# Optimization experiments

Hardware: AMD Instinct MI355X
Metric: run time of the kernel (lower is better)

## Reference

```python
import jax, jax.numpy as jnp
import numpy as np

S, L, K = 4, 256, 32          # num_states, seq length, neighbors
ORIG_H, EMB_H, EXV, RANK = 128, 256, 384, 16


def _integrate(x, Wq, Wk, seq_idx, emb_idx, hidden, rank):
    """AttentionIntegrator.forward: QK^T softmax -> double mean -> softmax -> weighted pool of raw x."""
    x = jnp.moveaxis(x, (seq_idx, emb_idx), (-2, -1))
    orig_shape = x.shape
    Ls = orig_shape[-2]
    xf = x.reshape(-1, Ls, hidden)               # (B, Ls, hidden)
    B = xf.shape[0]
    q = (xf @ Wq.T).reshape(B, Ls, rank, hidden)  # head_dim == hidden
    k = (xf @ Wk.T).reshape(B, Ls, rank, hidden)
    scale = 1.0 / jnp.sqrt(jnp.asarray(hidden, xf.dtype))
    scores = jnp.einsum('blhd,bmhd->bhlm', q, k) * scale
    attn = jax.nn.softmax(scores, axis=-1)        # (B, rank, Ls, Ls)
    w = jax.nn.softmax(attn.mean(axis=(1, 2)), axis=-1)  # (B, Ls)
    pooled = jnp.einsum('bl,bld->bd', w, xf)      # (B, hidden)
    return (pooled.reshape(*orig_shape[:-2], hidden),
            w.reshape(*orig_shape[:-2], Ls))


def setup_inputs() -> dict:
    key = jax.random.key(0)
    ks = jax.random.split(key, 12)
    sc = lambda fan_in: 1.0 / np.sqrt(fan_in)
    return {
        'h_V':    jax.random.normal(ks[0], (S, L, ORIG_H), jnp.float32),
        'h_EXV':  jax.random.normal(ks[1], (S, L, K, EXV), jnp.float32),
        'W_hV':   jax.random.normal(ks[2], (EMB_H, ORIG_H), jnp.float32) * sc(ORIG_H),
        'b_hV':   jnp.zeros((EMB_H,), jnp.float32),
        'Wq_hv':  jax.random.normal(ks[3], (RANK * EMB_H, EMB_H), jnp.float32) * sc(EMB_H),
        'Wk_hv':  jax.random.normal(ks[4], (RANK * EMB_H, EMB_H), jnp.float32) * sc(EMB_H),
        'Wq_ce':  jax.random.normal(ks[5], (RANK * EXV, EXV), jnp.float32) * sc(EXV),
        'Wk_ce':  jax.random.normal(ks[6], (RANK * EXV, EXV), jnp.float32) * sc(EXV),
        'W_ce':   jax.random.normal(ks[7], (EMB_H, EXV), jnp.float32) * sc(EXV),
        'b_ce':   jnp.zeros((EMB_H,), jnp.float32),
        'Wq_sce': jax.random.normal(ks[8], (RANK * EMB_H, EMB_H), jnp.float32) * sc(EMB_H),
        'Wk_sce': jax.random.normal(ks[9], (RANK * EMB_H, EMB_H), jnp.float32) * sc(EMB_H),
    }


def reference(h_V, h_EXV, W_hV, b_hV, Wq_hv, Wk_hv, Wq_ce, Wk_ce, W_ce, b_ce, Wq_sce, Wk_sce):
    # diffmodel.get_weights
    hv = h_V @ W_hV.T + b_hV                                  # (S, L, EMB_H)
    h_V_int, h_V_w = _integrate(hv, Wq_hv, Wk_hv, 0, 2, EMB_H, RANK)   # pool over states
    # chemical environment: pool over k neighbors per (state, position)
    ce, _local_w = _integrate(h_EXV, Wq_ce, Wk_ce, 2, 3, EXV, RANK)    # (S, L, EXV)
    ce = ce @ W_ce.T + b_ce                                   # (S, L, EMB_H)
    ce_int, ce_w = _integrate(ce, Wq_sce, Wk_sce, 0, 2, EMB_H, RANK)   # pool over states
    return (h_V_int[None], h_V_w[None], ce_int[None], ce_w[None])
```

## Files before the change

kernel.cpp:

```cpp
#include <hip/hip_runtime.h>

typedef _Float16 f16;
typedef _Float16 f16x8 __attribute__((ext_vector_type(8)));
typedef _Float16 f16x4 __attribute__((ext_vector_type(4)));
typedef float f32x4 __attribute__((ext_vector_type(4)));

#define MFMA16(a, b, c) __builtin_amdgcn_mfma_f32_16x16x32_f16(a, b, c, 0, 0, 0)
#define MFMA16K16(a, b, c) __builtin_amdgcn_mfma_f32_16x16x16f16(a, b, c, 0, 0, 0)

__global__ __launch_bounds__(256) void k_mt(const float* __restrict__ Wq,
                                            const float* __restrict__ Wk,
                                            f16* __restrict__ MT, int H) {
    const int h = blockIdx.x;
    const int ntile = H >> 6;
    const int nkk = H >> 5;
    const int frow = (blockIdx.y / ntile) * 64;
    const int ecol = (blockIdx.y % ntile) * 64;
    const int t = threadIdx.x;
    const int lane = t & 63;
    const int w = t >> 6;
    const int wr = w >> 1, wc = w & 1;

    __shared__ __align__(16) f16 As[64][40];
    __shared__ __align__(16) f16 Ks[64][40];

    f32x4 acc[2][2] = {};
    const int d = t >> 3;
    const int e8 = (t & 7) * 8;

    for (int kk = 0; kk < nkk; ++kk) {
        const float* gq = Wq + (size_t)(h * H + kk * 32 + d) * H + ecol + e8;
        const float* gk = Wk + (size_t)(h * H + kk * 32 + d) * H + frow + e8;
        float q[8], k[8];
#pragma unroll
        for (int i = 0; i < 8; ++i) { q[i] = gq[i]; k[i] = gk[i]; }
        __syncthreads();
#pragma unroll
        for (int i = 0; i < 8; ++i) { As[e8 + i][d] = (f16)q[i]; Ks[e8 + i][d] = (f16)k[i]; }
        __syncthreads();
        f16x8 a[2], b[2];
#pragma unroll
        for (int rt = 0; rt < 2; ++rt)
            a[rt] = *(const f16x8*)&Ks[wr * 32 + rt * 16 + (lane & 15)][(lane >> 4) * 8];
#pragma unroll
        for (int nt = 0; nt < 2; ++nt)
            b[nt] = *(const f16x8*)&As[wc * 32 + nt * 16 + (lane & 15)][(lane >> 4) * 8];
#pragma unroll
        for (int rt = 0; rt < 2; ++rt)
#pragma unroll
            for (int nt = 0; nt < 2; ++nt)
                acc[rt][nt] = MFMA16(a[rt], b[nt], acc[rt][nt]);
    }
#pragma unroll
    for (int rt = 0; rt < 2; ++rt)
#pragma unroll
        for (int nt = 0; nt < 2; ++nt)
#pragma unroll
            for (int j = 0; j < 4; ++j) {
                int f = frow + wr * 32 + rt * 16 + (lane >> 4) * 4 + j;
                int e = ecol + wc * 32 + nt * 16 + (lane & 15);
                MT[(((size_t)h * nkk + (e >> 5)) * H + f) * 32 + (e & 31)] = (f16)acc[rt][nt][j];
            }
}

__global__ __launch_bounds__(256) void k_lin(const float* __restrict__ in,
                                             const float* __restrict__ W,
                                             const float* __restrict__ bias,
                                             float* __restrict__ out, int K) {
    const int t = threadIdx.x;
    const int r0 = blockIdx.x * 4;
    __shared__ float ins[4][384];
    __shared__ float Ws[256][33];
#pragma unroll
    for (int r = 0; r < 4; ++r)
        for (int off = t; off < K; off += 256)
            ins[r][off] = in[(size_t)(r0 + r) * K + off];
    float acc[4] = {};
    for (int d0 = 0; d0 < K; d0 += 32) {
        __syncthreads();
        for (int i = t; i < 256 * 32; i += 256) {
            int j = i >> 5, dd = i & 31;
            Ws[j][dd] = W[(size_t)j * K + d0 + dd];
        }
        __syncthreads();
#pragma unroll 8
        for (int dd = 0; dd < 32; ++dd) {
            float wv = Ws[t][dd];
#pragma unroll
            for (int r = 0; r < 4; ++r) acc[r] += wv * ins[r][d0 + dd];
        }
    }
    float bv = bias[t];
#pragma unroll
    for (int r = 0; r < 4; ++r) out[(size_t)(r0 + r) * 256 + t] = acc[r] + bv;
}

__global__ __launch_bounds__(256) void k_small_int(const float* __restrict__ X,
                                                   const f16* __restrict__ MT,
                                                   float* __restrict__ wpart) {
    const int t = threadIdx.x;
    const int lane = t & 63;
    const int w = t >> 6;
    const int g = lane >> 4;
    const int l15 = lane & 15;
    const int pos0 = blockIdx.x * 4;
    const int h = blockIdx.y;

    __shared__ __align__(16) f16 Xs[16][264];
    __shared__ __align__(16) f16 Ts[16][264];

    {
        int row = t >> 4, d0 = (t & 15) * 16;
        int s = row & 3, p = row >> 2;
        const float* gx = X + (size_t)(s * 256 + pos0 + p) * 256 + d0;
#pragma unroll
        for (int i = 0; i < 16; i += 8) {
            float4 v0 = *(const float4*)(gx + i);
            float4 v1 = *(const float4*)(gx + i + 4);
            f16x8 o;
            o[0] = (f16)v0.x; o[1] = (f16)v0.y; o[2] = (f16)v0.z; o[3] = (f16)v0.w;
            o[4] = (f16)v1.x; o[5] = (f16)v1.y; o[6] = (f16)v1.z; o[7] = (f16)v1.w;
            *(f16x8*)&Xs[row][d0 + i] = o;
        }
    }
    __syncthreads();

    const f16* mh = MT + (size_t)h * 8 * 256 * 32;
    const int fb = w * 64 + l15;
    f32x4 acc[4] = {};
    f16x8 bq[4], bn[4];
#pragma unroll
    for (int nt = 0; nt < 4; ++nt)
        bq[nt] = *(const f16x8*)(mh + (size_t)(fb + nt * 16) * 32 + g * 8);
#pragma unroll
    for (int kk = 0; kk < 8; ++kk) {
        if (kk < 7) {
#pragma unroll
            for (int nt = 0; nt < 4; ++nt)
                bn[nt] = *(const f16x8*)(mh + ((size_t)(kk + 1) * 256 + fb + nt * 16) * 32 + g * 8);
        }
        f16x8 a = *(const f16x8*)&Xs[l15][kk * 32 + g * 8];
#pragma unroll
        for (int nt = 0; nt < 4; ++nt) acc[nt] = MFMA16(a, bq[nt], acc[nt]);
#pragma unroll
        for (int nt = 0; nt < 4; ++nt) bq[nt] = bn[nt];
    }
#pragma unroll
    for (int nt = 0; nt < 4; ++nt)
#pragma unroll
        for (int j = 0; j < 4; ++j)
            Ts[g * 4 + j][w * 64 + nt * 16 + l15] = (f16)acc[nt][j];
    __syncthreads();

    f32x4 sacc = {};
#pragma unroll
    for (int ks = 0; ks < 8; ++ks) {
        f16x8 a = *(const f16x8*)&Ts[l15][ks * 32 + g * 8];
        f16x8 b = *(const f16x8*)&Xs[l15][ks * 32 + g * 8];
        sacc = MFMA16(a, b, sacc);
    }
    if (w == 0 && (l15 >> 2) == g) {
        const float scale = 1.0f / 16.0f;
        float add = 0.f;
#pragma unroll
        for (int j = 0; j < 4; ++j) {
            float v = sacc[j] * scale;
            float m = v;
            m = fmaxf(m, __shfl_xor(m, 1));
            m = fmaxf(m, __shfl_xor(m, 2));
            float e = expf(v - m);
            float s2 = e;
            s2 += __shfl_xor(s2, 1);
            s2 += __shfl_xor(s2, 2);
            add += e / s2;
        }
        int pg = pos0 + g;
        wpart[((size_t)h * 256 + pg) * 4 + (l15 & 3)] = add;
    }
}

__global__ __launch_bounds__(256) void k_small_fin(const float* __restrict__ wpart,
                                                   const float* __restrict__ X,
                                                   float* __restrict__ out_int,
                                                   float* __restrict__ out_w) {
    const int pos = blockIdx.x, t = threadIdx.x;
    __shared__ float red[64];
    __shared__ float ws[4];
    if (t < 64) red[t] = wpart[((size_t)(t >> 2) * 256 + pos) * 4 + (t & 3)];
    __syncthreads();
    if (t == 0) {
        float v[4];
#pragma unroll
        for (int s = 0; s < 4; ++s) {
            float x = 0.f;
            for (int hh = 0; hh < 16; ++hh) x += red[hh * 4 + s];
            v[s] = x * (1.0f / 64.0f);
        }
        float m = fmaxf(fmaxf(v[0], v[1]), fmaxf(v[2], v[3]));
        float sum = 0.f;
#pragma unroll
        for (int s = 0; s < 4; ++s) { v[s] = expf(v[s] - m); sum += v[s]; }
#pragma unroll
        for (int s = 0; s < 4; ++s) ws[s] = v[s] / sum;
    }
    __syncthreads();
    if (t < 4) out_w[pos * 4 + t] = ws[t];
    float v = 0.f;
#pragma unroll
    for (int s = 0; s < 4; ++s) v += ws[s] * X[(size_t)(s * 256 + pos) * 256 + t];
    out_int[(size_t)pos * 256 + t] = v;
}

#define BUF_OFF 98304

__global__ __launch_bounds__(512, 2) void k_ce_int(const float* __restrict__ Xg32,
                                                   const f16* __restrict__ MT,
                                                   float* __restrict__ acc_out) {
    const int t = threadIdx.x;
    const int lane = t & 63;
    const int w = t >> 6;
    const int g = lane >> 4;
    const int l15 = lane & 15;
    const int bg = blockIdx.x;

    extern __shared__ __align__(16) char smem[];
    char* BUF = smem + BUF_OFF;

    {
        const float* xg = Xg32 + (size_t)bg * 128 * 384;
#pragma unroll
        for (int p = 0; p < 12; ++p) {
            int idx = p * 512 + t;
            int row = idx / 48, s = idx - row * 48;
            int c = s ^ (row & 7);
            const float* src = xg + row * 384 + c * 8;
            float4 v0 = *(const float4*)src;
            float4 v1 = *(const float4*)(src + 4);
            f16x8 o;
            o[0] = (f16)v0.x; o[1] = (f16)v0.y; o[2] = (f16)v0.z; o[3] = (f16)v0.w;
            o[4] = (f16)v1.x; o[5] = (f16)v1.y; o[6] = (f16)v1.z; o[7] = (f16)v1.w;
            *(f16x8*)(smem + idx * 16) = o;
        }
    }
    __syncthreads();

    const f16* mall = MT;
    const int frow = w * 48 + l15;

    f16x8 A[3][3];
#pragma unroll
    for (int ft = 0; ft < 3; ++ft) {
        A[0][ft] = *(const f16x8*)(mall + (size_t)(frow + ft * 16) * 32 + g * 8);
        A[1][ft] = *(const f16x8*)(mall + (size_t)12288 + (size_t)(frow + ft * 16) * 32 + g * 8);
    }

    for (int hi = 0; hi < 16; ++hi) {
        f32x4 acc[3][8] = {};
#pragma unroll
        for (int kk = 0; kk < 12; ++kk) {
            {
                int step = hi * 12 + kk + 2;
                int ns = step < 192 ? step : 191;
#pragma unroll
                for (int ft = 0; ft < 3; ++ft)
                    A[(kk + 2) % 3][ft] =
                        *(const f16x8*)(mall + (size_t)ns * 12288 + (size_t)(frow + ft * 16) * 32 + g * 8);
            }
            f16x8 xb[8];
#pragma unroll
            for (int mt = 0; mt < 8; ++mt) {
                int row = mt * 16 + l15;
                int ch = kk * 4 + g;
                xb[mt] = *(const f16x8*)(smem + row * 768 + ((ch ^ (row & 7)) << 4));
            }
            __builtin_amdgcn_s_setprio(1);
#pragma unroll
            for (int ft = 0; ft < 3; ++ft)
#pragma unroll
                for (int mt = 0; mt < 8; ++mt)
                    acc[ft][mt] = MFMA16(A[kk % 3][ft], xb[mt], acc[ft][mt]);
            __builtin_amdgcn_s_setprio(0);
        }

        f16x4 bf[3][8];
#pragma unroll
        for (int ft = 0; ft < 3; ++ft)
#pragma unroll
            for (int mt = 0; mt < 8; ++mt) {
                f32x4 v = acc[ft][mt];
                f16x4 o;
                o[0] = (f16)v[0]; o[1] = (f16)v[1]; o[2] = (f16)v[2]; o[3] = (f16)v[3];
                bf[ft][mt] = o;
            }

#pragma unroll
        for (int r = 0; r < 2; ++r) {
            f32x4 s2[2][2][2] = {};
#pragma unroll
            for (int bb = 0; bb < 2; ++bb) {
                const int b = 2 * r + bb;
#pragma unroll
                for (int ks = 0; ks < 3; ++ks)
#pragma unroll
                    for (int it = 0; it < 2; ++it) {
                        int row = b * 32 + it * 16 + l15;
                        int ch = 6 * w + 2 * ks + (g >> 1);
                        f16x4 av = *(const f16x4*)(smem + row * 768 +
                                                   ((ch ^ (row & 7)) << 4) + 8 * (g & 1));
#pragma unroll
                        for (int lt = 0; lt < 2; ++lt)
                            s2[bb][it][lt] = MFMA16K16(av, bf[ks][2 * b + lt], s2[bb][it][lt]);
                    }
            }
#pragma unroll
            for (int bb = 0; bb < 2; ++bb)
#pragma unroll
                for (int it = 0; it < 2; ++it)
#pragma unroll
                    for (int lt = 0; lt < 2; ++lt)
                        *(f32x4*)(BUF + w * 8192 + (bb * 4 + it * 2 + lt) * 1024 + lane * 16) =
                            s2[bb][it][lt];
            __syncthreads();

            if ((w >> 2) == r) {
                const int wl = w & 3;
                const int bb = wl >> 1;
                const int it = wl & 1;
                const int b = 2 * r + bb;
                f32x4 sum0 = {0.f, 0.f, 0.f, 0.f};
                f32x4 sum1 = {0.f, 0.f, 0.f, 0.f};
#pragma unroll
                for (int src = 0; src < 8; ++src) {
                    const char* pb = BUF + src * 8192 + (bb * 4 + it * 2) * 1024 + lane * 16;
                    sum0 += *(const f32x4*)pb;
                    sum1 += *(const f32x4*)(pb + 1024);
                }
                const float scale = 0.051031036307982884f;
                float cs0 = 0.f, cs1 = 0.f;
#pragma unroll
                for (int j = 0; j < 4; ++j) {
                    float v0 = sum0[j] * scale, v1 = sum1[j] * scale;
                    float m = fmaxf(v0, v1);
                    m = fmaxf(m, __shfl_xor(m, 1));
                    m = fmaxf(m, __shfl_xor(m, 2));
                    m = fmaxf(m, __shfl_xor(m, 4));
                    m = fmaxf(m, __shfl_xor(m, 8));
                    float e0 = expf(v0 - m), e1 = expf(v1 - m);
                    float s = e0 + e1;
                    s += __shfl_xor(s, 1);
                    s += __shfl_xor(s, 2);
                    s += __shfl_xor(s, 4);
                    s += __shfl_xor(s, 8);
                    float inv = 1.f / s;
                    cs0 += e0 * inv;
                    cs1 += e1 * inv;
                }
                cs0 += __shfl_xor(cs0, 16); cs0 += __shfl_xor(cs0, 32);
                cs1 += __shfl_xor(cs1, 16); cs1 += __shfl_xor(cs1, 32);
                if (lane < 16) {
                    float* o = acc_out + (((size_t)hi * 1024 + bg * 4 + b) * 2 + it) * 32;
                    o[l15] = cs0;
                    o[16 + l15] = cs1;
                }
            }
            __syncthreads();
        }
    }
}

__global__ __launch_bounds__(128) void k_ce_pool(const float* __restrict__ accp,
                                                 const float* __restrict__ exv,
                                                 float* __restrict__ pooled) {
    const int b = blockIdx.x;
    const int t = threadIdx.x;
    __shared__ float wm[32];
    __shared__ float ww[32];
    if (t < 32) {
        float s = 0.f;
#pragma unroll
        for (int h = 0; h < 16; ++h) {
            s += accp[(((size_t)h * 1024 + b) * 2 + 0) * 32 + t];
            s += accp[(((size_t)h * 1024 + b) * 2 + 1) * 32 + t];
        }
        wm[t] = s * (1.0f / 512.0f);
    }
    __syncthreads();
    if (t == 0) {
        float m = wm[0];
        for (int i = 1; i < 32; ++i) m = fmaxf(m, wm[i]);
        float s = 0.f;
        for (int i = 0; i < 32; ++i) { float e = expf(wm[i] - m); ww[i] = e; s += e; }
        float inv = 1.f / s;
        for (int i = 0; i < 32; ++i) ww[i] *= inv;
    }
    __syncthreads();
    for (int d = t; d < 384; d += 128) {
        float v = 0.f;
#pragma unroll
        for (int m = 0; m < 32; ++m) v += ww[m] * exv[((size_t)b * 32 + m) * 384 + d];
        pooled[(size_t)b * 384 + d] = v;
    }
}

extern "C" void kernel_launch(void* const* d_in, const int* in_sizes, int n_in,
                              void* d_out, int out_size, void* d_ws, size_t ws_size,
                              hipStream_t stream) {
    const float* h_V    = (const float*)d_in[0];
    const float* h_EXV  = (const float*)d_in[1];
    const float* W_hV   = (const float*)d_in[2];
    const float* b_hV   = (const float*)d_in[3];
    const float* Wq_hv  = (const float*)d_in[4];
    const float* Wk_hv  = (const float*)d_in[5];
    const float* Wq_ce  = (const float*)d_in[6];
    const float* Wk_ce  = (const float*)d_in[7];
    const float* W_ce   = (const float*)d_in[8];
    const float* b_ce   = (const float*)d_in[9];
    const float* Wq_sce = (const float*)d_in[10];
    const float* Wk_sce = (const float*)d_in[11];
    float* out = (float*)d_out;

    char* ws = (char*)d_ws;
    f16*   mt_hv  = (f16*)(ws + 0);
    f16*   mt_sce = (f16*)(ws + 2097152);
    f16*   mt_ce  = (f16*)(ws + 4194304);
    float* hv     = (float*)(ws + 8912896);
    float* ce     = (float*)(ws + 9961472);
    float* accp   = (float*)(ws + 11010048);
    float* pooled = (float*)(ws + 15204352);
    float* wpart  = accp;

    k_mt<<<dim3(16, 16), 256, 0, stream>>>(Wq_hv, Wk_hv, mt_hv, 256);
    k_mt<<<dim3(16, 36), 256, 0, stream>>>(Wq_ce, Wk_ce, mt_ce, 384);
    k_mt<<<dim3(16, 16), 256, 0, stream>>>(Wq_sce, Wk_sce, mt_sce, 256);
    k_lin<<<256, 256, 0, stream>>>(h_V, W_hV, b_hV, hv, 128);
    k_small_int<<<dim3(64, 16), 256, 0, stream>>>(hv, mt_hv, wpart);
    k_small_fin<<<256, 256, 0, stream>>>(wpart, hv, out + 0, out + 65536);
    k_ce_int<<<dim3(256), 512, 163840, stream>>>(h_EXV, mt_ce, accp);
    k_ce_pool<<<1024, 128, 0, stream>>>(accp, h_EXV, pooled);
    k_lin<<<256, 256, 0, stream>>>(pooled, W_ce, b_ce, ce, 384);
    k_small_int<<<dim3(64, 16), 256, 0, stream>>>(ce, mt_sce, wpart);
    k_small_fin<<<256, 256, 0, stream>>>(wpart, ce, out + 66560, out + 132096);
}
```

Before: 318.7 us.

## Halve ce_int block work to 2 groups per block and merge MT kernels

The chemical-environment attention kernel now handles 64 rows (two neighbour groups) per block instead of 128, doubling the grid to 512 blocks and halving shared memory to 80 KB. This is meant to improve occupancy and load balance on the many CUs and raise the number of resident blocks. The cost is that each block reloads the full MT matrix stream for half the work, which doubles global/L2 traffic for MT. The three weight-product kernels are also merged into a single launch to cut launch overhead.

```diff
diff --git a/kernel.cpp b/kernel.cpp
--- a/kernel.cpp
+++ b/kernel.cpp
@@ -8,14 +8,28 @@
 #define MFMA16(a, b, c) __builtin_amdgcn_mfma_f32_16x16x32_f16(a, b, c, 0, 0, 0)
 #define MFMA16K16(a, b, c) __builtin_amdgcn_mfma_f32_16x16x16f16(a, b, c, 0, 0, 0)
 
-__global__ __launch_bounds__(256) void k_mt(const float* __restrict__ Wq,
-                                            const float* __restrict__ Wk,
-                                            f16* __restrict__ MT, int H) {
+__global__ __launch_bounds__(256) void k_mt3(const float* __restrict__ Wq_hv,
+                                             const float* __restrict__ Wk_hv,
+                                             f16* __restrict__ mt_hv,
+                                             const float* __restrict__ Wq_ce,
+                                             const float* __restrict__ Wk_ce,
+                                             f16* __restrict__ mt_ce,
+                                             const float* __restrict__ Wq_sce,
+                                             const float* __restrict__ Wk_sce,
+                                             f16* __restrict__ mt_sce) {
+    const int y = blockIdx.y;
+    const float *Wq, *Wk;
+    f16* MT;
+    int H, ty;
+    if (y < 16)      { Wq = Wq_hv;  Wk = Wk_hv;  MT = mt_hv;  H = 256; ty = y; }
+    else if (y < 52) { Wq = Wq_ce;  Wk = Wk_ce;  MT = mt_ce;  H = 384; ty = y - 16; }
+    else             { Wq = Wq_sce; Wk = Wk_sce; MT = mt_sce; H = 256; ty = y - 52; }
+
     const int h = blockIdx.x;
     const int ntile = H >> 6;
     const int nkk = H >> 5;
-    const int frow = (blockIdx.y / ntile) * 64;
-    const int ecol = (blockIdx.y % ntile) * 64;
+    const int frow = (ty / ntile) * 64;
+    const int ecol = (ty % ntile) * 64;
     const int t = threadIdx.x;
     const int lane = t & 63;
     const int w = t >> 6;
@@ -211,7 +225,7 @@
     out_int[(size_t)pos * 256 + t] = v;
 }
 
-#define BUF_OFF 98304
+#define BUF_OFF 49152
 
 __global__ __launch_bounds__(512, 2) void k_ce_int(const float* __restrict__ Xg32,
                                                    const f16* __restrict__ MT,
@@ -227,9 +241,9 @@
     char* BUF = smem + BUF_OFF;
 
     {
-        const float* xg = Xg32 + (size_t)bg * 128 * 384;
-#pragma unroll
-        for (int p = 0; p < 12; ++p) {
+        const float* xg = Xg32 + (size_t)bg * 64 * 384;
+#pragma unroll
+        for (int p = 0; p < 6; ++p) {
             int idx = p * 512 + t;
             int row = idx / 48, s = idx - row * 48;
             int c = s ^ (row & 7);
@@ -255,7 +269,7 @@
     }
 
     for (int hi = 0; hi < 16; ++hi) {
-        f32x4 acc[3][8] = {};
+        f32x4 acc[3][4] = {};
 #pragma unroll
         for (int kk = 0; kk < 12; ++kk) {
             {
@@ -266,9 +280,9 @@
                     A[(kk + 2) % 3][ft] =
                         *(const f16x8*)(mall + (size_t)ns * 12288 + (size_t)(frow + ft * 16) * 32 + g * 8);
             }
-            f16x8 xb[8];
-#pragma unroll
-            for (int mt = 0; mt < 8; ++mt) {
+            f16x8 xb[4];
+#pragma unroll
+            for (int mt = 0; mt < 4; ++mt) {
                 int row = mt * 16 + l15;
                 int ch = kk * 4 + g;
                 xb[mt] = *(const f16x8*)(smem + row * 768 + ((ch ^ (row & 7)) << 4));
@@ -277,16 +291,16 @@
 #pragma unroll
             for (int ft = 0; ft < 3; ++ft)
 #pragma unroll
-                for (int mt = 0; mt < 8; ++mt)
+                for (int mt = 0; mt < 4; ++mt)
                     acc[ft][mt] = MFMA16(A[kk % 3][ft], xb[mt], acc[ft][mt]);
             __builtin_amdgcn_s_setprio(0);
         }
 
-        f16x4 bf[3][8];
+        f16x4 bf[3][4];
 #pragma unroll
         for (int ft = 0; ft < 3; ++ft)
 #pragma unroll
-            for (int mt = 0; mt < 8; ++mt) {
+            for (int mt = 0; mt < 4; ++mt) {
                 f32x4 v = acc[ft][mt];
                 f16x4 o;
                 o[0] = (f16)v[0]; o[1] = (f16)v[1]; o[2] = (f16)v[2]; o[3] = (f16)v[3];
@@ -295,43 +309,32 @@
 
 #pragma unroll
         for (int r = 0; r < 2; ++r) {
-            f32x4 s2[2][2][2] = {};
-#pragma unroll
-            for (int bb = 0; bb < 2; ++bb) {
-                const int b = 2 * r + bb;
-#pragma unroll
-                for (int ks = 0; ks < 3; ++ks)
-#pragma unroll
-                    for (int it = 0; it < 2; ++it) {
-                        int row = b * 32 + it * 16 + l15;
-                        int ch = 6 * w + 2 * ks + (g >> 1);
-                        f16x4 av = *(const f16x4*)(smem + row * 768 +
-                                                   ((ch ^ (row & 7)) << 4) + 8 * (g & 1));
-#pragma unroll
-                        for (int lt = 0; lt < 2; ++lt)
-                            s2[bb][it][lt] = MFMA16K16(av, bf[ks][2 * b + lt], s2[bb][it][lt]);
-                    }
-            }
-#pragma unroll
-            for (int bb = 0; bb < 2; ++bb)
-#pragma unroll
-                for (int it = 0; it < 2; ++it)
+            f32x4 s2[2][2] = {};
+#pragma unroll
+            for (int ks = 0; ks < 3; ++ks)
+#pragma unroll
+                for (int it = 0; it < 2; ++it) {
+                    int row = r * 32 + it * 16 + l15;
+                    int ch = 6 * w + 2 * ks + (g >> 1);
+                    f16x4 av = *(const f16x4*)(smem + row * 768 +
+                                               ((ch ^ (row & 7)) << 4) + 8 * (g & 1));
 #pragma unroll
                     for (int lt = 0; lt < 2; ++lt)
-                        *(f32x4*)(BUF + w * 8192 + (bb * 4 + it * 2 + lt) * 1024 + lane * 16) =
-                            s2[bb][it][lt];
+                        s2[it][lt] = MFMA16K16(av, bf[ks][r * 2 + lt], s2[it][lt]);
+                }
+#pragma unroll
+            for (int it = 0; it < 2; ++it)
+#pragma unroll
+                for (int lt = 0; lt < 2; ++lt)
+                    *(f32x4*)(BUF + w * 4096 + (it * 2 + lt) * 1024 + lane * 16) = s2[it][lt];
             __syncthreads();
 
-            if ((w >> 2) == r) {
-                const int wl = w & 3;
-                const int bb = wl >> 1;
-                const int it = wl & 1;
-                const int b = 2 * r + bb;
+            if (w < 2) {
                 f32x4 sum0 = {0.f, 0.f, 0.f, 0.f};
                 f32x4 sum1 = {0.f, 0.f, 0.f, 0.f};
 #pragma unroll
                 for (int src = 0; src < 8; ++src) {
-                    const char* pb = BUF + src * 8192 + (bb * 4 + it * 2) * 1024 + lane * 16;
+                    const char* pb = BUF + src * 4096 + (w * 2) * 1024 + lane * 16;
                     sum0 += *(const f32x4*)pb;
                     sum1 += *(const f32x4*)(pb + 1024);
                 }
@@ -358,7 +361,7 @@
                 cs0 += __shfl_xor(cs0, 16); cs0 += __shfl_xor(cs0, 32);
                 cs1 += __shfl_xor(cs1, 16); cs1 += __shfl_xor(cs1, 32);
                 if (lane < 16) {
-                    float* o = acc_out + (((size_t)hi * 1024 + bg * 4 + b) * 2 + it) * 32;
+                    float* o = acc_out + (((size_t)hi * 1024 + bg * 2 + r) * 2 + w) * 32;
                     o[l15] = cs0;
                     o[16 + l15] = cs1;
                 }
@@ -429,13 +432,13 @@
     float* pooled = (float*)(ws + 15204352);
     float* wpart  = accp;
 
-    k_mt<<<dim3(16, 16), 256, 0, stream>>>(Wq_hv, Wk_hv, mt_hv, 256);
-    k_mt<<<dim3(16, 36), 256, 0, stream>>>(Wq_ce, Wk_ce, mt_ce, 384);
-    k_mt<<<dim3(16, 16), 256, 0, stream>>>(Wq_sce, Wk_sce, mt_sce, 256);
+    k_mt3<<<dim3(16, 68), 256, 0, stream>>>(Wq_hv, Wk_hv, mt_hv,
+                                            Wq_ce, Wk_ce, mt_ce,
+                                            Wq_sce, Wk_sce, mt_sce);
     k_lin<<<256, 256, 0, stream>>>(h_V, W_hV, b_hV, hv, 128);
     k_small_int<<<dim3(64, 16), 256, 0, stream>>>(hv, mt_hv, wpart);
     k_small_fin<<<256, 256, 0, stream>>>(wpart, hv, out + 0, out + 65536);
-    k_ce_int<<<dim3(256), 512, 163840, stream>>>(h_EXV, mt_ce, accp);
+    k_ce_int<<<dim3(512), 512, 81920, stream>>>(h_EXV, mt_ce, accp);
     k_ce_pool<<<1024, 128, 0, stream>>>(accp, h_EXV, pooled);
     k_lin<<<256, 256, 0, stream>>>(pooled, W_ce, b_ce, ce, 384);
     k_small_int<<<dim3(64, 16), 256, 0, stream>>>(ce, mt_sce, wpart);
```

Result: slower. 376.9 us (+18.3%).
